# Performance work log

Measured on AMD Instinct MI355X. Metric: run time of the kernel, lower is better.

Reference implementation:

```python
import jax, jax.numpy as jnp
import numpy as np

EPS_LN = 1e-6


def _ln(x):
    m = jnp.mean(x, axis=-1, keepdims=True)
    v = jnp.mean((x - m) ** 2, axis=-1, keepdims=True)
    return (x - m) * jax.lax.rsqrt(v + EPS_LN)


def _rope(q, cos, sin):
    # q: [B,S,H,D]; cos/sin: [S, D//2]; rotate interleaved pairs
    q2 = q.reshape(q.shape[:-1] + (-1, 2))
    a, b = q2[..., 0], q2[..., 1]
    c = cos[None, :, None, :]
    s = sin[None, :, None, :]
    return jnp.stack([a * c - b * s, a * s + b * c], axis=-1).reshape(q.shape)


def _attn(q, k, v):
    # q:[B,Sq,H,D] k,v:[B,Sk,H,D] -> [B,Sq,H,D]; flash default scale 1/sqrt(D)
    D = q.shape[-1]
    scores = jnp.einsum('bqhd,bkhd->bhqk', q, k) / jnp.sqrt(jnp.asarray(D, q.dtype))
    p = jax.nn.softmax(scores, axis=-1)
    return jnp.einsum('bhqk,bkhd->bqhd', p, v)


def setup_inputs() -> dict:
    key = jax.random.key(0)
    C, H, S, T, B = 2048, 16, 1024, 256, 4
    Dh = C // H
    F = int(C * 4)
    L, Ly = B * S, B * T
    ks = jax.random.split(key, 24)

    def w(k, shape):
        return (jax.random.normal(k, shape, dtype=jnp.float32) * 0.02)

    # RoPE angle table: positions 0..S-1 with standard inverse frequencies
    inv_freq = 1.0 / (10000.0 ** (np.arange(0, Dh, 2, dtype=np.float32) / Dh))
    freqs = jnp.asarray(np.arange(S, dtype=np.float32)[:, None] * inv_freq[None, :])

    inp = {
        'x': jax.random.normal(ks[0], (L, C), dtype=jnp.float32),
        'y': jax.random.normal(ks[1], (Ly, C), dtype=jnp.float32),
        't': jax.random.normal(ks[2], (L, 6 * C), dtype=jnp.float32),
        'freqs': freqs,
        'scale_shift_table': jax.random.normal(ks[3], (6, C), dtype=jnp.float32) / (C ** 0.5),
        'Wq_s': w(ks[4], (C, C)), 'bq_s': jnp.zeros((C,), jnp.float32),
        'Wk_s': w(ks[5], (C, C)), 'bk_s': jnp.zeros((C,), jnp.float32),
        'Wv_s': w(ks[6], (C, C)), 'bv_s': jnp.zeros((C,), jnp.float32),
        'Wo_s': w(ks[7], (C, C)), 'bo_s': jnp.zeros((C,), jnp.float32),
        'Wq_c': w(ks[8], (C, C)), 'bq_c': jnp.zeros((C,), jnp.float32),
        'Wk_c': w(ks[9], (C, C)), 'bk_c': jnp.zeros((C,), jnp.float32),
        'Wv_c': w(ks[10], (C, C)), 'bv_c': jnp.zeros((C,), jnp.float32),
        'Wo_c': w(ks[11], (C, C)), 'bo_c': jnp.zeros((C,), jnp.float32),
        'W_fc1': w(ks[12], (F, C)), 'b_fc1': jnp.zeros((F,), jnp.float32),
        'W_fc2': w(ks[13], (C, F)), 'b_fc2': jnp.zeros((C,), jnp.float32),
        'seq_len': S,
        'txt_len': T,
    }
    return inp


def reference(x, y, t, freqs, scale_shift_table,
              Wq_s, bq_s, Wk_s, bk_s, Wv_s, bv_s, Wo_s, bo_s,
              Wq_c, bq_c, Wk_c, bk_c, Wv_c, bv_c, Wo_c, bo_c,
              W_fc1, b_fc1, W_fc2, b_fc2, seq_len, txt_len):
    L, C = x.shape
    Dh = 2 * freqs.shape[1]
    H = C // Dh
    B = L // seq_len
    cos, sin = jnp.cos(freqs), jnp.sin(freqs)

    # per-token AdaLN params (B here == total tokens in torch code)
    mods = scale_shift_table[None] + t.reshape(L, 6, C)
    shift_msa, scale_msa, gate_msa, shift_mlp, scale_mlp, gate_mlp = (
        mods[:, i, :] for i in range(6))

    # ---- self attention (AdaLN modulate + RoPE) ----
    xm = _ln(x) * (1.0 + scale_msa) + shift_msa
    q = (xm @ Wq_s.T + bq_s).reshape(B, seq_len, H, Dh)
    k = (xm @ Wk_s.T + bk_s).reshape(B, seq_len, H, Dh)
    v = (xm @ Wv_s.T + bv_s).reshape(B, seq_len, H, Dh)
    q = _rope(q, cos, sin)
    k = _rope(k, cos, sin)
    a = _attn(q, k, v).reshape(L, C)
    x = x + gate_msa * (a @ Wo_s.T + bo_s)

    # ---- cross attention (no norm/modulation/gate, no RoPE) ----
    q = (x @ Wq_c.T + bq_c).reshape(B, seq_len, H, Dh)
    k = (y @ Wk_c.T + bk_c).reshape(B, txt_len, H, Dh)
    v = (y @ Wv_c.T + bv_c).reshape(B, txt_len, H, Dh)
    a = _attn(q, k, v).reshape(L, C)
    x = x + (a @ Wo_c.T + bo_c)

    # ---- MLP with AdaLN modulate + gate ----
    xm = _ln(x) * (1.0 + scale_mlp) + shift_mlp
    h = jax.nn.gelu(xm @ W_fc1.T + b_fc1, approximate=True)
    x = x + gate_mlp * (h @ W_fc2.T + b_fc2)
    return x
```

## Files before the change

### kernel.cpp

```cpp
#include <hip/hip_runtime.h>
#include <stdint.h>

#define C_DIM 2048
#define H_NUM 16
#define DH    128
#define S_LEN 1024
#define T_LEN 256
#define B_SZ  4
#define L_ROWS 4096
#define LY_ROWS 1024
#define F_DIM 8192

typedef __attribute__((ext_vector_type(4))) float f32x4;
typedef __attribute__((ext_vector_type(8))) __bf16 bf16x8;
typedef __attribute__((ext_vector_type(4))) unsigned short us4;
typedef __attribute__((ext_vector_type(8))) unsigned short us8;
typedef unsigned short u16;

__device__ __forceinline__ u16 f2bf(float f) {
  union { float f; uint32_t u; } v; v.f = f;
  uint32_t r = v.u + 0x7FFFu + ((v.u >> 16) & 1u);
  return (u16)(r >> 16);
}
__device__ __forceinline__ float bf2f(u16 h) {
  union { uint32_t u; float f; } v; v.u = ((uint32_t)h) << 16;
  return v.f;
}

typedef __attribute__((address_space(1))) void gvoid;
typedef __attribute__((address_space(3))) void lvoid;
__device__ __forceinline__ void gl_lds16(const void* g, void* l) {
  __builtin_amdgcn_global_load_lds((gvoid*)g, (lvoid*)l, 16, 0, 0);
}

template<int N> __device__ __forceinline__ void wait_vmcnt() {
  if constexpr (N == 0) asm volatile("s_waitcnt vmcnt(0)" ::: "memory");
  else if constexpr (N == 5) asm volatile("s_waitcnt vmcnt(5)" ::: "memory");
  else if constexpr (N == 6) asm volatile("s_waitcnt vmcnt(6)" ::: "memory");
}
__device__ __forceinline__ void barrier_raw() {
  asm volatile("s_barrier" ::: "memory");
}
__device__ __forceinline__ void lgkm0_pin() {
  asm volatile("s_waitcnt lgkmcnt(0)" ::: "memory");
  __builtin_amdgcn_sched_barrier(0);
}

__global__ void k_cvt(const float* __restrict__ src, u16* __restrict__ dst, int n) {
  int i = (blockIdx.x * blockDim.x + threadIdx.x) * 4;
  int stride = gridDim.x * blockDim.x * 4;
  for (; i < n; i += stride) {
    float4 v = *(const float4*)(src + i);
    us4 o;
    o[0] = f2bf(v.x); o[1] = f2bf(v.y); o[2] = f2bf(v.z); o[3] = f2bf(v.w);
    *(us4*)(dst + i) = o;
  }
}

__global__ __launch_bounds__(256)
void k_modln(const float* __restrict__ x, const float* __restrict__ t,
             const float* __restrict__ tab, u16* __restrict__ out,
             int scale_idx, int shift_idx) {
  int row = blockIdx.x;
  int tid = threadIdx.x;
  const float* xr = x + (size_t)row * C_DIM;
  int c0 = tid * 8;
  float4 a = *(const float4*)(xr + c0);
  float4 b = *(const float4*)(xr + c0 + 4);
  float v[8] = {a.x, a.y, a.z, a.w, b.x, b.y, b.z, b.w};
  float s = 0.f, ss = 0.f;
#pragma unroll
  for (int j = 0; j < 8; ++j) { s += v[j]; ss += v[j] * v[j]; }
#pragma unroll
  for (int m = 1; m < 64; m <<= 1) { s += __shfl_xor(s, m); ss += __shfl_xor(ss, m); }
  __shared__ float red[8];
  int wid = tid >> 6;
  if ((tid & 63) == 0) { red[wid * 2] = s; red[wid * 2 + 1] = ss; }
  __syncthreads();
  s  = red[0] + red[2] + red[4] + red[6];
  ss = red[1] + red[3] + red[5] + red[7];
  float mean = s * (1.f / C_DIM);
  float var  = ss * (1.f / C_DIM) - mean * mean;
  float rstd = rsqrtf(var + 1e-6f);
  const float* trow = t + (size_t)row * (6 * C_DIM);
  const float* tsc = trow + scale_idx * C_DIM + c0;
  const float* tsh = trow + shift_idx * C_DIM + c0;
  const float* gsc = tab + scale_idx * C_DIM + c0;
  const float* gsh = tab + shift_idx * C_DIM + c0;
  us8 o;
#pragma unroll
  for (int j = 0; j < 8; ++j) {
    float scv = 1.f + gsc[j] + tsc[j];
    float shv = gsh[j] + tsh[j];
    o[j] = f2bf((v[j] - mean) * rstd * scv + shv);
  }
  *(us8*)(out + (size_t)row * C_DIM + c0) = o;
}

template<int BM, int EPI>
__global__ __launch_bounds__(512, 2)
void k_gemm3(const u16* __restrict__ A, const u16* __restrict__ W,
             const float* __restrict__ bias0, const float* __restrict__ bias1,
             const float* __restrict__ bias2,
             u16* __restrict__ o0, u16* __restrict__ o1, u16* __restrict__ o2,
             int sec_shift, int out_ld,
             float* __restrict__ outF, const float* __restrict__ resid,
             const float* __restrict__ gate_t, const float* __restrict__ gate_tab,
             int M, int N, int K, int nbx) {
  constexpr int HTA = (BM / 2) * 64;
  constexpr int HTB = 128 * 64;
  constexpr int ACALLS = BM / 128;
  constexpr int QM = BM / 64;
  constexpr int MFR = BM / 32;
  constexpr int VMN = 4 + ACALLS;
  constexpr int BOFF = 4 * HTA;
  __shared__ __align__(16) u16 lds[BOFF + 4 * HTB];

  int tid = threadIdx.x;
  int nwg = gridDim.x;
  int q8 = nwg >> 3, r8 = nwg & 7;
  int xcd = blockIdx.x & 7, local = blockIdx.x >> 3;
  int wgid = (xcd < r8 ? xcd * (q8 + 1) : r8 * (q8 + 1) + (xcd - r8) * q8) + local;
  int bx = wgid % nbx, by = wgid / nbx;
  int m0 = by * BM, n0 = bx * 256;

  int wid = tid >> 6, lane = tid & 63;
  int wm = wid >> 2, wn = wid & 3;
  int lr = lane & 15, lg = lane >> 4;
  int xorslot = ((lr >> 2) & 3) << 1;
  int bcol = (wn & 1) * 64;

  int tsw = tid ^ (((tid >> 5) & 1) << 1) ^ (((tid >> 6) & 1) << 2);
  int srow = tsw >> 3;
  int scol = (tsw & 7) * 8;

  auto stA = [&](int h, int kt2) {
    int pt = kt2 & 1;
    u16* dst = lds + (pt * 2 + h) * HTA + tid * 8;
#pragma unroll
    for (int call = 0; call < ACALLS; ++call) {
      int grow = m0 + h * (BM / 2) + call * 64 + srow;
      gl_lds16(A + (size_t)grow * K + kt2 * 64 + scol, dst + call * 4096);
    }
  };
  auto stB = [&](int h, int kt2) {
    int pt = kt2 & 1;
    u16* dst = lds + BOFF + (pt * 2 + h) * HTB + tid * 8;
#pragma unroll
    for (int call = 0; call < 2; ++call) {
      int grow = n0 + h * 128 + call * 64 + srow;
      gl_lds16(W + (size_t)grow * K + kt2 * 64 + scol, dst + call * 4096);
    }
  };

  f32x4 zero4 = {0.f, 0.f, 0.f, 0.f};
  f32x4 acc[MFR][4];
#pragma unroll
  for (int m = 0; m < MFR; ++m)
#pragma unroll
    for (int n = 0; n < 4; ++n) acc[m][n] = zero4;

  int NT2 = K >> 6;
  stA(0, 0); stA(1, 0); stB(0, 0); stB(1, 0);
  stB(0, 1); stB(1, 1); stA(0, 1);
  wait_vmcnt<VMN>();
  barrier_raw();

  for (int kt = 0; kt < NT2; ++kt) {
    int p = kt & 1;
    const u16* Ah = lds + (p * 2 + wm) * HTA;
    const u16* Bh = lds + BOFF + (p * 2 + (wn >> 1)) * HTB;
    bf16x8 aR[QM][2], bR0[2][2], bR1[2][2];
    bool st1 = (kt + 1) < NT2, st2 = (kt + 2) < NT2;

#pragma unroll
    for (int m = 0; m < QM; ++m) {
      int r = m * 16 + lr;
#pragma unroll
      for (int kk = 0; kk < 2; ++kk)
        aR[m][kk] = *(const bf16x8*)(Ah + r * 64 + (((kk << 2) | lg) ^ xorslot) * 8);
    }
#pragma unroll
    for (int n = 0; n < 2; ++n) {
      int r = bcol + n * 16 + lr;
#pragma unroll
      for (int kk = 0; kk < 2; ++kk)
        bR0[n][kk] = *(const bf16x8*)(Bh + r * 64 + (((kk << 2) | lg) ^ xorslot) * 8);
    }
    if (st1) stA(1, kt + 1);
    lgkm0_pin();
    __builtin_amdgcn_s_setprio(1);
#pragma unroll
    for (int kk = 0; kk < 2; ++kk)
#pragma unroll
      for (int m = 0; m < QM; ++m)
#pragma unroll
        for (int n = 0; n < 2; ++n)
          acc[m][n] = __builtin_amdgcn_mfma_f32_16x16x32_bf16(aR[m][kk], bR0[n][kk], acc[m][n], 0, 0, 0);
    __builtin_amdgcn_s_setprio(0);
    barrier_raw();

#pragma unroll
    for (int n = 0; n < 2; ++n) {
      int r = bcol + 32 + n * 16 + lr;
#pragma unroll
      for (int kk = 0; kk < 2; ++kk)
        bR1[n][kk] = *(const bf16x8*)(Bh + r * 64 + (((kk << 2) | lg) ^ xorslot) * 8);
    }
    lgkm0_pin();
    __builtin_amdgcn_s_setprio(1);
#pragma unroll
    for (int kk = 0; kk < 2; ++kk)
#pragma unroll
      for (int m = 0; m < QM; ++m)
#pragma unroll
        for (int n = 0; n < 2; ++n)
          acc[m][2 + n] = __builtin_amdgcn_mfma_f32_16x16x32_bf16(aR[m][kk], bR1[n][kk], acc[m][2 + n], 0, 0, 0);
    __builtin_amdgcn_s_setprio(0);
    barrier_raw();

#pragma unroll
    for (int m = 0; m < QM; ++m) {
      int r = (BM / 4) + m * 16 + lr;
#pragma unroll
      for (int kk = 0; kk < 2; ++kk)
        aR[m][kk] = *(const bf16x8*)(Ah + r * 64 + (((kk << 2) | lg) ^ xorslot) * 8);
    }
    if (st2) { stB(0, kt + 2); stB(1, kt + 2); }
    lgkm0_pin();
    __builtin_amdgcn_s_setprio(1);
#pragma unroll
    for (int kk = 0; kk < 2; ++kk)
#pragma unroll
      for (int m = 0; m < QM; ++m)
#pragma unroll
        for (int n = 0; n < 2; ++n)
          acc[QM + m][2 + n] = __builtin_amdgcn_mfma_f32_16x16x32_bf16(aR[m][kk], bR1[n][kk], acc[QM + m][2 + n], 0, 0, 0);
    __builtin_amdgcn_s_setprio(0);
    barrier_raw();

    if (st2) stA(0, kt + 2);
    __builtin_amdgcn_s_setprio(1);
#pragma unroll
    for (int kk = 0; kk < 2; ++kk)
#pragma unroll
      for (int m = 0; m < QM; ++m)
#pragma unroll
        for (int n = 0; n < 2; ++n)
          acc[QM + m][n] = __builtin_amdgcn_mfma_f32_16x16x32_bf16(aR[m][kk], bR0[n][kk], acc[QM + m][n], 0, 0, 0);
    __builtin_amdgcn_s_setprio(0);
    if (st2) wait_vmcnt<VMN>(); else wait_vmcnt<0>();
    barrier_raw();
  }

#pragma unroll
  for (int mf = 0; mf < MFR; ++mf) {
    int row0 = m0 + wm * (BM / 2) + mf * 16 + lg * 4;
#pragma unroll
    for (int nf = 0; nf < 4; ++nf) {
      int col = n0 + wn * 64 + nf * 16 + lr;
      if constexpr (EPI == 0) {
        int sec = col >> sec_shift;
        const float* bp = sec == 0 ? bias0 : (sec == 1 ? bias1 : bias2);
        u16* op = sec == 0 ? o0 : (sec == 1 ? o1 : o2);
        int cs = col & ((1 << sec_shift) - 1);
        float bv = bp[cs];
#pragma unroll
        for (int r = 0; r < 4; ++r)
          op[(size_t)(row0 + r) * out_ld + cs] = f2bf(acc[mf][nf][r] + bv);
      } else if constexpr (EPI == 1) {
        float bv = bias0[col];
#pragma unroll
        for (int r = 0; r < 4; ++r) {
          float val = acc[mf][nf][r] + bv;
          float x3 = val * val * val;
          float g = 0.5f * val * (1.f + tanhf(0.7978845608f * (val + 0.044715f * x3)));
          o0[(size_t)(row0 + r) * out_ld + col] = f2bf(g);
        }
      } else if constexpr (EPI == 2) {
        float bv = bias0[col];
        float gt = gate_tab[col];
#pragma unroll
        for (int r = 0; r < 4; ++r) {
          int row = row0 + r;
          size_t idx = (size_t)row * N + col;
          float g = gt + gate_t[(size_t)row * (6 * C_DIM) + col];
          float o = resid[idx] + g * (acc[mf][nf][r] + bv);
          outF[idx] = o;
          if (o0) o0[idx] = f2bf(o);
        }
      } else {
        float bv = bias0[col];
#pragma unroll
        for (int r = 0; r < 4; ++r) {
          size_t idx = (size_t)(row0 + r) * N + col;
          outF[idx] = resid[idx] + (acc[mf][nf][r] + bv);
        }
      }
    }
  }
}

__global__ void k_rope(u16* __restrict__ q, u16* __restrict__ k,
                       const float* __restrict__ freqs) {
  int idx = blockIdx.x * blockDim.x + threadIdx.x;
  int total = L_ROWS * C_DIM / 8;
  for (; idx < total; idx += gridDim.x * blockDim.x) {
    int e = idx * 8;
    int row = e >> 11;
    int col = e & (C_DIM - 1);
    int s = row & (S_LEN - 1);
    int i0 = (col & (DH - 1)) >> 1;
    float4 fr = *(const float4*)(freqs + s * (DH / 2) + i0);
    float cs[4], sn[4];
    float fv[4] = {fr.x, fr.y, fr.z, fr.w};
#pragma unroll
    for (int j = 0; j < 4; ++j) sincosf(fv[j], &sn[j], &cs[j]);
    us8 qa = *(us8*)(q + e);
    us8 ka = *(us8*)(k + e);
#pragma unroll
    for (int p = 0; p < 4; ++p) {
      float a = bf2f(qa[2 * p]), b = bf2f(qa[2 * p + 1]);
      qa[2 * p]     = f2bf(a * cs[p] - b * sn[p]);
      qa[2 * p + 1] = f2bf(a * sn[p] + b * cs[p]);
      float a2 = bf2f(ka[2 * p]), b2 = bf2f(ka[2 * p + 1]);
      ka[2 * p]     = f2bf(a2 * cs[p] - b2 * sn[p]);
      ka[2 * p + 1] = f2bf(a2 * sn[p] + b2 * cs[p]);
    }
    *(us8*)(q + e) = qa;
    *(us8*)(k + e) = ka;
  }
}

__global__ void k_transpose_v(const u16* __restrict__ v, u16* __restrict__ vt, int Lkv) {
  __shared__ u16 tile[32][33];
  int bh = blockIdx.x, b = bh >> 4, h = bh & 15;
  int k0 = blockIdx.y * 32, d0 = blockIdx.z * 32;
  int tx = threadIdx.x, ty = threadIdx.y;
  const u16* src = v + (size_t)(b * Lkv) * C_DIM + h * DH;
#pragma unroll
  for (int j = 0; j < 32; j += 8)
    tile[ty + j][tx] = src[(size_t)(k0 + ty + j) * C_DIM + d0 + tx];
  __syncthreads();
  u16* dst = vt + (size_t)bh * DH * Lkv;
#pragma unroll
  for (int j = 0; j < 32; j += 8)
    dst[(size_t)(d0 + ty + j) * Lkv + k0 + tx] = tile[tx][ty + j];
}

__global__ __launch_bounds__(256)
void k_flash(const u16* __restrict__ Q, const u16* __restrict__ K,
             const u16* __restrict__ Vt, u16* __restrict__ O,
             int Lq, int Lkv, float scale) {
  __shared__ __align__(16) u16 lK[64 * 128];
  __shared__ __align__(16) u16 lV[128 * 64];
  __shared__ __align__(16) u16 lP[4][16 * 72];
  int bh = blockIdx.x, b = bh >> 4, h = bh & 15;
  int tid = threadIdx.x, wid = tid >> 6, lane = tid & 63;
  int lr = lane & 15, lg = lane >> 4;
  int q0 = blockIdx.y * 64 + wid * 16;
  const u16* Qb = Q + ((size_t)(b * Lq) + q0) * C_DIM + h * DH;
  const u16* Kb = K + (size_t)(b * Lkv) * C_DIM + h * DH;
  const u16* Vb = Vt + (size_t)bh * DH * Lkv;

  bf16x8 qf[4];
#pragma unroll
  for (int ks = 0; ks < 4; ++ks)
    qf[ks] = *(const bf16x8*)(Qb + (size_t)lr * C_DIM + ks * 32 + lg * 8);

  f32x4 zero4 = {0.f, 0.f, 0.f, 0.f};
  f32x4 o[8];
#pragma unroll
  for (int n = 0; n < 8; ++n) o[n] = zero4;
  float mrow[4] = {-3.0e38f, -3.0e38f, -3.0e38f, -3.0e38f};
  float lrow[4] = {0.f, 0.f, 0.f, 0.f};

  int nsteps = Lkv >> 6;
  for (int kt = 0; kt < nsteps; ++kt) {
#pragma unroll
    for (int i = 0; i < 4; ++i) {
      int flat = i * 4096 + tid * 16;
      int key = flat >> 8, inner = flat & 255;
      int ksrc = inner ^ ((key & 7) << 4);
      gl_lds16((const char*)Kb + ((size_t)(kt * 64 + key) * C_DIM) * 2 + ksrc, (char*)lK + flat);
      int d = flat >> 7, keyb = flat & 127;
      int vsrc = keyb ^ ((d & 7) << 4);
      gl_lds16((const char*)Vb + ((size_t)d * Lkv) * 2 + kt * 128 + vsrc, (char*)lV + flat);
    }
    __syncthreads();

    f32x4 sc[4];
#pragma unroll
    for (int c = 0; c < 4; ++c) sc[c] = zero4;
#pragma unroll
    for (int c = 0; c < 4; ++c) {
      int key = c * 16 + lr;
#pragma unroll
      for (int ks = 0; ks < 4; ++ks) {
        int off = (ks * 64 + lg * 16) ^ ((key & 7) << 4);
        bf16x8 kf = *(const bf16x8*)((const char*)lK + key * 256 + off);
        sc[c] = __builtin_amdgcn_mfma_f32_16x16x32_bf16(qf[ks], kf, sc[c], 0, 0, 0);
      }
    }
#pragma unroll
    for (int r = 0; r < 4; ++r) {
      float s0 = sc[0][r] * scale, s1 = sc[1][r] * scale;
      float s2 = sc[2][r] * scale, s3 = sc[3][r] * scale;
      float mx = fmaxf(fmaxf(s0, s1), fmaxf(s2, s3));
#pragma unroll
      for (int m = 1; m < 16; m <<= 1) mx = fmaxf(mx, __shfl_xor(mx, m));
      float mnew = fmaxf(mrow[r], mx);
      float alpha = exp2f((mrow[r] - mnew) * 1.44269504f);
      mrow[r] = mnew;
      float p0 = exp2f((s0 - mnew) * 1.44269504f);
      float p1 = exp2f((s1 - mnew) * 1.44269504f);
      float p2 = exp2f((s2 - mnew) * 1.44269504f);
      float p3 = exp2f((s3 - mnew) * 1.44269504f);
      float psum = p0 + p1 + p2 + p3;
#pragma unroll
      for (int m = 1; m < 16; m <<= 1) psum += __shfl_xor(psum, m);
      lrow[r] = lrow[r] * alpha + psum;
#pragma unroll
      for (int n = 0; n < 8; ++n) o[n][r] *= alpha;
      u16* pr = lP[wid] + (4 * lg + r) * 72;
      pr[lr]      = f2bf(p0);
      pr[16 + lr] = f2bf(p1);
      pr[32 + lr] = f2bf(p2);
      pr[48 + lr] = f2bf(p3);
    }
    asm volatile("s_waitcnt lgkmcnt(0)" ::: "memory");
    __builtin_amdgcn_sched_barrier(0);
#pragma unroll
    for (int half = 0; half < 2; ++half) {
      bf16x8 pf = *(const bf16x8*)(lP[wid] + lr * 72 + half * 32 + lg * 8);
#pragma unroll
      for (int n = 0; n < 8; ++n) {
        int d = n * 16 + lr;
        int off = (half * 64 + lg * 16) ^ ((d & 7) << 4);
        bf16x8 vf = *(const bf16x8*)((const char*)lV + d * 128 + off);
        o[n] = __builtin_amdgcn_mfma_f32_16x16x32_bf16(pf, vf, o[n], 0, 0, 0);
      }
    }
    __syncthreads();
  }

  u16* Ob = O + ((size_t)(b * Lq) + q0) * C_DIM + h * DH;
#pragma unroll
  for (int n = 0; n < 8; ++n) {
    int d = n * 16 + lr;
#pragma unroll
    for (int r = 0; r < 4; ++r) {
      int qr = 4 * lg + r;
      Ob[(size_t)qr * C_DIM + d] = f2bf(o[n][r] / lrow[r]);
    }
  }
}

extern "C" void kernel_launch(void* const* d_in, const int* in_sizes, int n_in,
                              void* d_out, int out_size, void* d_ws, size_t ws_size,
                              hipStream_t stream) {
  const float* x     = (const float*)d_in[0];
  const float* y     = (const float*)d_in[1];
  const float* t     = (const float*)d_in[2];
  const float* freqs = (const float*)d_in[3];
  const float* tab   = (const float*)d_in[4];
  const float* Wq_s = (const float*)d_in[5];
  const float* bq_s = (const float*)d_in[6];
  const float* Wk_s = (const float*)d_in[7];
  const float* bk_s = (const float*)d_in[8];
  const float* Wv_s = (const float*)d_in[9];
  const float* bv_s = (const float*)d_in[10];
  const float* Wo_s = (const float*)d_in[11];
  const float* bo_s = (const float*)d_in[12];
  const float* Wq_c = (const float*)d_in[13];
  const float* bq_c = (const float*)d_in[14];
  const float* Wk_c = (const float*)d_in[15];
  const float* bk_c = (const float*)d_in[16];
  const float* Wv_c = (const float*)d_in[17];
  const float* bv_c = (const float*)d_in[18];
  const float* Wo_c = (const float*)d_in[19];
  const float* bo_c = (const float*)d_in[20];
  const float* W_fc1 = (const float*)d_in[21];
  const float* b_fc1 = (const float*)d_in[22];
  const float* W_fc2 = (const float*)d_in[23];
  const float* b_fc2 = (const float*)d_in[24];

  const size_t SZ_CC  = (size_t)C_DIM * C_DIM * 2;
  const size_t SZ_FC  = (size_t)F_DIM * C_DIM * 2;
  const size_t SZ_LC  = (size_t)L_ROWS * C_DIM * 2;
  const size_t SZ_YC  = (size_t)LY_ROWS * C_DIM * 2;
  char* ws = (char*)d_ws;
  size_t off = 0;
  u16* wq_s = (u16*)(ws + off); off += SZ_CC;
  u16* wk_s = (u16*)(ws + off); off += SZ_CC;
  u16* wv_s = (u16*)(ws + off); off += SZ_CC;
  u16* wo_s = (u16*)(ws + off); off += SZ_CC;
  u16* wq_c = (u16*)(ws + off); off += SZ_CC;
  u16* wk_c = (u16*)(ws + off); off += SZ_CC;
  u16* wv_c = (u16*)(ws + off); off += SZ_CC;
  u16* wo_c = (u16*)(ws + off); off += SZ_CC;
  u16* wfc1 = (u16*)(ws + off); off += SZ_FC;
  u16* wfc2 = (u16*)(ws + off); off += SZ_FC;
  u16* ybf  = (u16*)(ws + off); off += SZ_YC;
  u16* xm   = (u16*)(ws + off); off += SZ_LC;
  u16* qb   = (u16*)(ws + off); off += SZ_LC;
  u16* kb   = (u16*)(ws + off); off += SZ_LC;
  u16* vb   = (u16*)(ws + off); off += SZ_LC;
  u16* ao   = (u16*)(ws + off); off += SZ_LC;
  u16* hbuf = qb;
  float* x1 = (float*)(ws + off); off += (size_t)L_ROWS * C_DIM * 4;
  u16* x1bf = (u16*)(ws + off); off += SZ_LC;
  u16* kc   = (u16*)(ws + off); off += SZ_YC;
  u16* vc   = (u16*)(ws + off); off += SZ_YC;
  u16* vt   = (u16*)(ws + off); off += SZ_LC;
  u16* vtc  = (u16*)(ws + off); off += SZ_YC;
  if (ws_size < off) return;

  auto cvt = [&](const float* s, u16* d, int n) {
    int blocks = (n / 4 + 255) / 256; if (blocks > 4096) blocks = 4096;
    k_cvt<<<blocks, 256, 0, stream>>>(s, d, n);
  };
  cvt(Wq_s, wq_s, C_DIM * C_DIM);
  cvt(Wk_s, wk_s, C_DIM * C_DIM);
  cvt(Wv_s, wv_s, C_DIM * C_DIM);
  cvt(Wo_s, wo_s, C_DIM * C_DIM);
  cvt(Wq_c, wq_c, C_DIM * C_DIM);
  cvt(Wk_c, wk_c, C_DIM * C_DIM);
  cvt(Wv_c, wv_c, C_DIM * C_DIM);
  cvt(Wo_c, wo_c, C_DIM * C_DIM);
  cvt(W_fc1, wfc1, F_DIM * C_DIM);
  cvt(W_fc2, wfc2, F_DIM * C_DIM);
  cvt(y, ybf, LY_ROWS * C_DIM);

  const float ascale = 0.08838834764831845f;

  k_modln<<<L_ROWS, 256, 0, stream>>>(x, t, tab, xm, 1, 0);
  k_gemm3<128, 0><<<32 * 24, 512, 0, stream>>>(
      xm, wq_s, bq_s, bk_s, bv_s, qb, kb, vb, 11, C_DIM,
      nullptr, nullptr, nullptr, nullptr, L_ROWS, 6144, C_DIM, 24);
  k_rope<<<2048, 256, 0, stream>>>(qb, kb, freqs);
  k_transpose_v<<<dim3(B_SZ * H_NUM, S_LEN / 32, DH / 32), dim3(32, 8), 0, stream>>>(vb, vt, S_LEN);
  k_flash<<<dim3(B_SZ * H_NUM, S_LEN / 64), 256, 0, stream>>>(qb, kb, vt, ao, S_LEN, S_LEN, ascale);
  k_gemm3<128, 2><<<32 * 8, 512, 0, stream>>>(
      ao, wo_s, bo_s, nullptr, nullptr, x1bf, nullptr, nullptr, 30, C_DIM,
      x1, x, t + 2 * C_DIM, tab + 2 * C_DIM, L_ROWS, C_DIM, C_DIM, 8);
  k_gemm3<128, 0><<<32 * 8, 512, 0, stream>>>(
      x1bf, wq_c, bq_c, nullptr, nullptr, qb, nullptr, nullptr, 30, C_DIM,
      nullptr, nullptr, nullptr, nullptr, L_ROWS, C_DIM, C_DIM, 8);
  k_gemm3<128, 0><<<8 * 16, 512, 0, stream>>>(
      ybf, wk_c, bk_c, bv_c, bv_c, kc, vc, vc, 11, C_DIM,
      nullptr, nullptr, nullptr, nullptr, LY_ROWS, 4096, C_DIM, 16);
  k_transpose_v<<<dim3(B_SZ * H_NUM, T_LEN / 32, DH / 32), dim3(32, 8), 0, stream>>>(vc, vtc, T_LEN);
  k_flash<<<dim3(B_SZ * H_NUM, S_LEN / 64), 256, 0, stream>>>(qb, kc, vtc, ao, S_LEN, T_LEN, ascale);
  k_gemm3<128, 3><<<32 * 8, 512, 0, stream>>>(
      ao, wo_c, bo_c, nullptr, nullptr, nullptr, nullptr, nullptr, 30, C_DIM,
      x1, x1, nullptr, nullptr, L_ROWS, C_DIM, C_DIM, 8);
  k_modln<<<L_ROWS, 256, 0, stream>>>(x1, t, tab, xm, 4, 3);
  k_gemm3<256, 1><<<16 * 32, 512, 0, stream>>>(
      xm, wfc1, b_fc1, nullptr, nullptr, hbuf, nullptr, nullptr, 30, F_DIM,
      nullptr, nullptr, nullptr, nullptr, L_ROWS, F_DIM, C_DIM, 32);
  k_gemm3<128, 2><<<32 * 8, 512, 0, stream>>>(
      hbuf, wfc2, b_fc2, nullptr, nullptr, nullptr, nullptr, nullptr, 30, C_DIM,
      (float*)d_out, x1, t + 5 * C_DIM, tab + 5 * C_DIM, L_ROWS, C_DIM, F_DIM, 8);
}
```

Baseline: 947.5 us.

## Split FC2 GEMM along K into two passes and change the LDS swizzle

```diff
diff --git a/kernel.cpp b/kernel.cpp
--- a/kernel.cpp
+++ b/kernel.cpp
@@ -106,7 +106,8 @@
              int sec_shift, int out_ld,
              float* __restrict__ outF, const float* __restrict__ resid,
              const float* __restrict__ gate_t, const float* __restrict__ gate_tab,
-             int M, int N, int K, int nbx) {
+             const float* __restrict__ partial,
+             int M, int N, int K, int lda, int ldw, int nbx) {
   constexpr int HTA = (BM / 2) * 64;
   constexpr int HTB = 128 * 64;
   constexpr int ACALLS = BM / 128;
@@ -127,12 +128,11 @@
   int wid = tid >> 6, lane = tid & 63;
   int wm = wid >> 2, wn = wid & 3;
   int lr = lane & 15, lg = lane >> 4;
-  int xorslot = ((lr >> 2) & 3) << 1;
+  int xorslot = lr & 7;
   int bcol = (wn & 1) * 64;
 
-  int tsw = tid ^ (((tid >> 5) & 1) << 1) ^ (((tid >> 6) & 1) << 2);
-  int srow = tsw >> 3;
-  int scol = (tsw & 7) * 8;
+  int srow = tid >> 3;
+  int scol = ((tid ^ (tid >> 3)) & 7) * 8;
 
   auto stA = [&](int h, int kt2) {
     int pt = kt2 & 1;
@@ -140,7 +140,7 @@
 #pragma unroll
     for (int call = 0; call < ACALLS; ++call) {
       int grow = m0 + h * (BM / 2) + call * 64 + srow;
-      gl_lds16(A + (size_t)grow * K + kt2 * 64 + scol, dst + call * 4096);
+      gl_lds16(A + (size_t)grow * lda + kt2 * 64 + scol, dst + call * 4096);
     }
   };
   auto stB = [&](int h, int kt2) {
@@ -149,7 +149,7 @@
 #pragma unroll
     for (int call = 0; call < 2; ++call) {
       int grow = n0 + h * 128 + call * 64 + srow;
-      gl_lds16(W + (size_t)grow * K + kt2 * 64 + scol, dst + call * 4096);
+      gl_lds16(W + (size_t)grow * ldw + kt2 * 64 + scol, dst + call * 4096);
     }
   };
 
@@ -178,14 +178,14 @@
       int r = m * 16 + lr;
 #pragma unroll
       for (int kk = 0; kk < 2; ++kk)
-        aR[m][kk] = *(const bf16x8*)(Ah + r * 64 + (((kk << 2) | lg) ^ xorslot) * 8);
+        aR[m][kk] = *(const bf16x8*)(Ah + r * 64 + ((((kk << 2) | lg) ^ xorslot)) * 8);
     }
 #pragma unroll
     for (int n = 0; n < 2; ++n) {
       int r = bcol + n * 16 + lr;
 #pragma unroll
       for (int kk = 0; kk < 2; ++kk)
-        bR0[n][kk] = *(const bf16x8*)(Bh + r * 64 + (((kk << 2) | lg) ^ xorslot) * 8);
+        bR0[n][kk] = *(const bf16x8*)(Bh + r * 64 + ((((kk << 2) | lg) ^ xorslot)) * 8);
     }
     if (st1) stA(1, kt + 1);
     lgkm0_pin();
@@ -205,7 +205,7 @@
       int r = bcol + 32 + n * 16 + lr;
 #pragma unroll
       for (int kk = 0; kk < 2; ++kk)
-        bR1[n][kk] = *(const bf16x8*)(Bh + r * 64 + (((kk << 2) | lg) ^ xorslot) * 8);
+        bR1[n][kk] = *(const bf16x8*)(Bh + r * 64 + ((((kk << 2) | lg) ^ xorslot)) * 8);
     }
     lgkm0_pin();
     __builtin_amdgcn_s_setprio(1);
@@ -224,7 +224,7 @@
       int r = (BM / 4) + m * 16 + lr;
 #pragma unroll
       for (int kk = 0; kk < 2; ++kk)
-        aR[m][kk] = *(const bf16x8*)(Ah + r * 64 + (((kk << 2) | lg) ^ xorslot) * 8);
+        aR[m][kk] = *(const bf16x8*)(Ah + r * 64 + ((((kk << 2) | lg) ^ xorslot)) * 8);
     }
     if (st2) { stB(0, kt + 2); stB(1, kt + 2); }
     lgkm0_pin();
@@ -289,12 +289,27 @@
           outF[idx] = o;
           if (o0) o0[idx] = f2bf(o);
         }
-      } else {
+      } else if constexpr (EPI == 3) {
         float bv = bias0[col];
 #pragma unroll
         for (int r = 0; r < 4; ++r) {
           size_t idx = (size_t)(row0 + r) * N + col;
           outF[idx] = resid[idx] + (acc[mf][nf][r] + bv);
+        }
+      } else if constexpr (EPI == 4) {
+#pragma unroll
+        for (int r = 0; r < 4; ++r)
+          outF[(size_t)(row0 + r) * N + col] = acc[mf][nf][r];
+      } else {
+        float bv = bias0[col];
+        float gt = gate_tab[col];
+#pragma unroll
+        for (int r = 0; r < 4; ++r) {
+          int row = row0 + r;
+          size_t idx = (size_t)row * N + col;
+          float val = acc[mf][nf][r] + partial[idx] + bv;
+          float g = gt + gate_t[(size_t)row * (6 * C_DIM) + col];
+          outF[idx] = resid[idx] + g * val;
         }
       }
     }
@@ -514,6 +529,7 @@
   u16* vc   = (u16*)(ws + off); off += SZ_YC;
   u16* vt   = (u16*)(ws + off); off += SZ_LC;
   u16* vtc  = (u16*)(ws + off); off += SZ_YC;
+  float* part = (float*)x1bf;
   if (ws_size < off) return;
 
   auto cvt = [&](const float* s, u16* d, int n) {
@@ -537,29 +553,33 @@
   k_modln<<<L_ROWS, 256, 0, stream>>>(x, t, tab, xm, 1, 0);
   k_gemm3<128, 0><<<32 * 24, 512, 0, stream>>>(
       xm, wq_s, bq_s, bk_s, bv_s, qb, kb, vb, 11, C_DIM,
-      nullptr, nullptr, nullptr, nullptr, L_ROWS, 6144, C_DIM, 24);
+      nullptr, nullptr, nullptr, nullptr, nullptr, L_ROWS, 6144, C_DIM, C_DIM, C_DIM, 24);
   k_rope<<<2048, 256, 0, stream>>>(qb, kb, freqs);
   k_transpose_v<<<dim3(B_SZ * H_NUM, S_LEN / 32, DH / 32), dim3(32, 8), 0, stream>>>(vb, vt, S_LEN);
   k_flash<<<dim3(B_SZ * H_NUM, S_LEN / 64), 256, 0, stream>>>(qb, kb, vt, ao, S_LEN, S_LEN, ascale);
   k_gemm3<128, 2><<<32 * 8, 512, 0, stream>>>(
       ao, wo_s, bo_s, nullptr, nullptr, x1bf, nullptr, nullptr, 30, C_DIM,
-      x1, x, t + 2 * C_DIM, tab + 2 * C_DIM, L_ROWS, C_DIM, C_DIM, 8);
+      x1, x, t + 2 * C_DIM, tab + 2 * C_DIM, nullptr, L_ROWS, C_DIM, C_DIM, C_DIM, C_DIM, 8);
   k_gemm3<128, 0><<<32 * 8, 512, 0, stream>>>(
       x1bf, wq_c, bq_c, nullptr, nullptr, qb, nullptr, nullptr, 30, C_DIM,
-      nullptr, nullptr, nullptr, nullptr, L_ROWS, C_DIM, C_DIM, 8);
+      nullptr, nullptr, nullptr, nullptr, nullptr, L_ROWS, C_DIM, C_DIM, C_DIM, C_DIM, 8);
   k_gemm3<128, 0><<<8 * 16, 512, 0, stream>>>(
       ybf, wk_c, bk_c, bv_c, bv_c, kc, vc, vc, 11, C_DIM,
-      nullptr, nullptr, nullptr, nullptr, LY_ROWS, 4096, C_DIM, 16);
+      nullptr, nullptr, nullptr, nullptr, nullptr, LY_ROWS, 4096, C_DIM, C_DIM, C_DIM, 16);
   k_transpose_v<<<dim3(B_SZ * H_NUM, T_LEN / 32, DH / 32), dim3(32, 8), 0, stream>>>(vc, vtc, T_LEN);
   k_flash<<<dim3(B_SZ * H_NUM, S_LEN / 64), 256, 0, stream>>>(qb, kc, vtc, ao, S_LEN, T_LEN, ascale);
   k_gemm3<128, 3><<<32 * 8, 512, 0, stream>>>(
       ao, wo_c, bo_c, nullptr, nullptr, nullptr, nullptr, nullptr, 30, C_DIM,
-      x1, x1, nullptr, nullptr, L_ROWS, C_DIM, C_DIM, 8);
+      x1, x1, nullptr, nullptr, nullptr, L_ROWS, C_DIM, C_DIM, C_DIM, C_DIM, 8);
   k_modln<<<L_ROWS, 256, 0, stream>>>(x1, t, tab, xm, 4, 3);
   k_gemm3<256, 1><<<16 * 32, 512, 0, stream>>>(
       xm, wfc1, b_fc1, nullptr, nullptr, hbuf, nullptr, nullptr, 30, F_DIM,
-      nullptr, nullptr, nullptr, nullptr, L_ROWS, F_DIM, C_DIM, 32);
-  k_gemm3<128, 2><<<32 * 8, 512, 0, stream>>>(
-      hbuf, wfc2, b_fc2, nullptr, nullptr, nullptr, nullptr, nullptr, 30, C_DIM,
-      (float*)d_out, x1, t + 5 * C_DIM, tab + 5 * C_DIM, L_ROWS, C_DIM, F_DIM, 8);
-}
+      nullptr, nullptr, nullptr, nullptr, nullptr, L_ROWS, F_DIM, C_DIM, C_DIM, C_DIM, 32);
+  k_gemm3<128, 4><<<32 * 8, 512, 0, stream>>>(
+      hbuf, wfc2, nullptr, nullptr, nullptr, nullptr, nullptr, nullptr, 30, C_DIM,
+      part, nullptr, nullptr, nullptr, nullptr, L_ROWS, C_DIM, F_DIM / 2, F_DIM, F_DIM, 8);
+  k_gemm3<128, 5><<<32 * 8, 512, 0, stream>>>(
+      hbuf + F_DIM / 2, wfc2 + F_DIM / 2, b_fc2, nullptr, nullptr, nullptr, nullptr, nullptr, 30, C_DIM,
+      (float*)d_out, x1, t + 5 * C_DIM, tab + 5 * C_DIM, part,
+      L_ROWS, C_DIM, F_DIM / 2, F_DIM, F_DIM, 8);
+}
```

Measured after the change: 917.9 us. 3.1% less time.

## Add 256x256 GEMM kernel with finer-grained load/MFMA interleaving for QKV and FC1

Applied to the files above, without the earlier changes.

```diff
diff --git a/kernel.cpp b/kernel.cpp
--- a/kernel.cpp
+++ b/kernel.cpp
@@ -35,6 +35,7 @@
 
 template<int N> __device__ __forceinline__ void wait_vmcnt() {
   if constexpr (N == 0) asm volatile("s_waitcnt vmcnt(0)" ::: "memory");
+  else if constexpr (N == 4) asm volatile("s_waitcnt vmcnt(4)" ::: "memory");
   else if constexpr (N == 5) asm volatile("s_waitcnt vmcnt(5)" ::: "memory");
   else if constexpr (N == 6) asm volatile("s_waitcnt vmcnt(6)" ::: "memory");
 }
@@ -97,6 +98,189 @@
   *(us8*)(out + (size_t)row * C_DIM + c0) = o;
 }
 
+template<int EPI>
+__global__ __launch_bounds__(512, 2)
+void k_gemm5(const u16* __restrict__ A, const u16* __restrict__ W,
+             const float* __restrict__ bias0, const float* __restrict__ bias1,
+             const float* __restrict__ bias2,
+             u16* __restrict__ o0, u16* __restrict__ o1, u16* __restrict__ o2,
+             int sec_shift, int out_ld,
+             int M, int N, int K, int lda, int ldw, int nbx) {
+  __shared__ __align__(16) u16 lds[65536];
+
+  int tid = threadIdx.x;
+  int nwg = gridDim.x;
+  int q8 = nwg >> 3, r8 = nwg & 7;
+  int xcd = blockIdx.x & 7, local = blockIdx.x >> 3;
+  int wgid = (xcd < r8 ? xcd * (q8 + 1) : r8 * (q8 + 1) + (xcd - r8) * q8) + local;
+  int bx = wgid % nbx, by = wgid / nbx;
+  int m0 = by * 256, n0 = bx * 256;
+
+  int wid = tid >> 6, lane = tid & 63;
+  int wm = wid >> 2, wn = wid & 3;
+  int lr = lane & 15, lg = lane >> 4;
+  int xorslot = lr & 7;
+  int bcol = (wn & 1) * 64;
+
+  int srow = tid >> 3;
+  int scol = ((tid ^ (tid >> 3)) & 7) * 8;
+
+  auto stA = [&](int buf, int h, int kt) {
+    u16* dst = lds + (buf * 2 + h) * 8192 + tid * 8;
+#pragma unroll
+    for (int call = 0; call < 2; ++call) {
+      int grow = m0 + h * 128 + call * 64 + srow;
+      gl_lds16(A + (size_t)grow * lda + kt * 64 + scol, dst + call * 4096);
+    }
+  };
+  auto stB = [&](int buf, int h, int kt) {
+    u16* dst = lds + 32768 + (buf * 2 + h) * 8192 + tid * 8;
+#pragma unroll
+    for (int call = 0; call < 2; ++call) {
+      int grow = n0 + h * 128 + call * 64 + srow;
+      gl_lds16(W + (size_t)grow * ldw + kt * 64 + scol, dst + call * 4096);
+    }
+  };
+
+  f32x4 zero4 = {0.f, 0.f, 0.f, 0.f};
+  f32x4 acc[8][4];
+#pragma unroll
+  for (int m = 0; m < 8; ++m)
+#pragma unroll
+    for (int n = 0; n < 4; ++n) acc[m][n] = zero4;
+
+  int NT = K >> 6, NJ = NT >> 1;
+  stA(0, 0, 0); stA(0, 1, 0); stB(0, 0, 0); stB(0, 1, 0);
+  stB(1, 0, 1); stA(1, 0, 1);
+  wait_vmcnt<4>();
+  barrier_raw();
+
+  for (int j = 0; j < NJ; ++j) {
+    bool nlast = (j + 1 < NJ);
+    int t1 = 2 * j + 1, t2 = 2 * j + 2, t3 = 2 * j + 3;
+#pragma unroll
+    for (int buf = 0; buf < 2; ++buf) {
+      const u16* Ah = lds + (buf * 2 + wm) * 8192;
+      const u16* Bh = lds + 32768 + (buf * 2 + (wn >> 1)) * 8192;
+      bf16x8 aR[4][2], b0[2][2], b1[2][2];
+
+#pragma unroll
+      for (int m = 0; m < 4; ++m) {
+        int r = m * 16 + lr;
+#pragma unroll
+        for (int kk = 0; kk < 2; ++kk)
+          aR[m][kk] = *(const bf16x8*)(Ah + r * 64 + (((kk << 2) | lg) ^ xorslot) * 8);
+      }
+#pragma unroll
+      for (int n = 0; n < 2; ++n) {
+        int r = bcol + n * 16 + lr;
+#pragma unroll
+        for (int kk = 0; kk < 2; ++kk)
+          b0[n][kk] = *(const bf16x8*)(Bh + r * 64 + (((kk << 2) | lg) ^ xorslot) * 8);
+      }
+      if (buf == 0) stA(1, 1, t1);
+      else if (nlast) stA(0, 1, t2);
+      barrier_raw();
+      lgkm0_pin();
+      __builtin_amdgcn_s_setprio(1);
+#pragma unroll
+      for (int kk = 0; kk < 2; ++kk)
+#pragma unroll
+        for (int m = 0; m < 4; ++m)
+#pragma unroll
+          for (int n = 0; n < 2; ++n)
+            acc[m][n] = __builtin_amdgcn_mfma_f32_16x16x32_bf16(aR[m][kk], b0[n][kk], acc[m][n], 0, 0, 0);
+      __builtin_amdgcn_s_setprio(0);
+      barrier_raw();
+
+#pragma unroll
+      for (int n = 0; n < 2; ++n) {
+        int r = bcol + 32 + n * 16 + lr;
+#pragma unroll
+        for (int kk = 0; kk < 2; ++kk)
+          b1[n][kk] = *(const bf16x8*)(Bh + r * 64 + (((kk << 2) | lg) ^ xorslot) * 8);
+      }
+      if (buf == 0) stB(1, 1, t1);
+      else if (nlast) stB(0, 1, t2);
+      barrier_raw();
+      lgkm0_pin();
+      __builtin_amdgcn_s_setprio(1);
+#pragma unroll
+      for (int kk = 0; kk < 2; ++kk)
+#pragma unroll
+        for (int m = 0; m < 4; ++m)
+#pragma unroll
+          for (int n = 0; n < 2; ++n)
+            acc[m][2 + n] = __builtin_amdgcn_mfma_f32_16x16x32_bf16(aR[m][kk], b1[n][kk], acc[m][2 + n], 0, 0, 0);
+      __builtin_amdgcn_s_setprio(0);
+      barrier_raw();
+
+#pragma unroll
+      for (int m = 0; m < 4; ++m) {
+        int r = 64 + m * 16 + lr;
+#pragma unroll
+        for (int kk = 0; kk < 2; ++kk)
+          aR[m][kk] = *(const bf16x8*)(Ah + r * 64 + (((kk << 2) | lg) ^ xorslot) * 8);
+      }
+      if (nlast) { if (buf == 0) stB(0, 0, t2); else stB(1, 0, t3); }
+      barrier_raw();
+      lgkm0_pin();
+      __builtin_amdgcn_s_setprio(1);
+#pragma unroll
+      for (int kk = 0; kk < 2; ++kk)
+#pragma unroll
+        for (int m = 0; m < 4; ++m)
+#pragma unroll
+          for (int n = 0; n < 2; ++n)
+            acc[4 + m][2 + n] = __builtin_amdgcn_mfma_f32_16x16x32_bf16(aR[m][kk], b1[n][kk], acc[4 + m][2 + n], 0, 0, 0);
+      __builtin_amdgcn_s_setprio(0);
+      barrier_raw();
+
+      if (nlast) { if (buf == 0) stA(0, 0, t2); else stA(1, 0, t3); }
+      barrier_raw();
+      __builtin_amdgcn_s_setprio(1);
+#pragma unroll
+      for (int kk = 0; kk < 2; ++kk)
+#pragma unroll
+        for (int m = 0; m < 4; ++m)
+#pragma unroll
+          for (int n = 0; n < 2; ++n)
+            acc[4 + m][n] = __builtin_amdgcn_mfma_f32_16x16x32_bf16(aR[m][kk], b0[n][kk], acc[4 + m][n], 0, 0, 0);
+      __builtin_amdgcn_s_setprio(0);
+      if (nlast) wait_vmcnt<4>(); else wait_vmcnt<0>();
+      barrier_raw();
+    }
+  }
+
+#pragma unroll
+  for (int mf = 0; mf < 8; ++mf) {
+    int row0 = m0 + wm * 128 + mf * 16 + lg * 4;
+#pragma unroll
+    for (int nf = 0; nf < 4; ++nf) {
+      int col = n0 + wn * 64 + nf * 16 + lr;
+      if constexpr (EPI == 0) {
+        int sec = col >> sec_shift;
+        const float* bp = sec == 0 ? bias0 : (sec == 1 ? bias1 : bias2);
+        u16* op = sec == 0 ? o0 : (sec == 1 ? o1 : o2);
+        int cs = col & ((1 << sec_shift) - 1);
+        float bv = bp[cs];
+#pragma unroll
+        for (int r = 0; r < 4; ++r)
+          op[(size_t)(row0 + r) * out_ld + cs] = f2bf(acc[mf][nf][r] + bv);
+      } else {
+        float bv = bias0[col];
+#pragma unroll
+        for (int r = 0; r < 4; ++r) {
+          float val = acc[mf][nf][r] + bv;
+          float x3 = val * val * val;
+          float g = 0.5f * val * (1.f + tanhf(0.7978845608f * (val + 0.044715f * x3)));
+          o0[(size_t)(row0 + r) * out_ld + col] = f2bf(g);
+        }
+      }
+    }
+  }
+}
+
 template<int BM, int EPI>
 __global__ __launch_bounds__(512, 2)
 void k_gemm3(const u16* __restrict__ A, const u16* __restrict__ W,
@@ -106,7 +290,7 @@
              int sec_shift, int out_ld,
              float* __restrict__ outF, const float* __restrict__ resid,
              const float* __restrict__ gate_t, const float* __restrict__ gate_tab,
-             int M, int N, int K, int nbx) {
+             int M, int N, int K, int lda, int ldw, int nbx) {
   constexpr int HTA = (BM / 2) * 64;
   constexpr int HTB = 128 * 64;
   constexpr int ACALLS = BM / 128;
@@ -127,12 +311,11 @@
   int wid = tid >> 6, lane = tid & 63;
   int wm = wid >> 2, wn = wid & 3;
   int lr = lane & 15, lg = lane >> 4;
-  int xorslot = ((lr >> 2) & 3) << 1;
+  int xorslot = lr & 7;
   int bcol = (wn & 1) * 64;
 
-  int tsw = tid ^ (((tid >> 5) & 1) << 1) ^ (((tid >> 6) & 1) << 2);
-  int srow = tsw >> 3;
-  int scol = (tsw & 7) * 8;
+  int srow = tid >> 3;
+  int scol = ((tid ^ (tid >> 3)) & 7) * 8;
 
   auto stA = [&](int h, int kt2) {
     int pt = kt2 & 1;
@@ -140,7 +323,7 @@
 #pragma unroll
     for (int call = 0; call < ACALLS; ++call) {
       int grow = m0 + h * (BM / 2) + call * 64 + srow;
-      gl_lds16(A + (size_t)grow * K + kt2 * 64 + scol, dst + call * 4096);
+      gl_lds16(A + (size_t)grow * lda + kt2 * 64 + scol, dst + call * 4096);
     }
   };
   auto stB = [&](int h, int kt2) {
@@ -149,7 +332,7 @@
 #pragma unroll
     for (int call = 0; call < 2; ++call) {
       int grow = n0 + h * 128 + call * 64 + srow;
-      gl_lds16(W + (size_t)grow * K + kt2 * 64 + scol, dst + call * 4096);
+      gl_lds16(W + (size_t)grow * ldw + kt2 * 64 + scol, dst + call * 4096);
     }
   };
 
@@ -268,15 +451,6 @@
 #pragma unroll
         for (int r = 0; r < 4; ++r)
           op[(size_t)(row0 + r) * out_ld + cs] = f2bf(acc[mf][nf][r] + bv);
-      } else if constexpr (EPI == 1) {
-        float bv = bias0[col];
-#pragma unroll
-        for (int r = 0; r < 4; ++r) {
-          float val = acc[mf][nf][r] + bv;
-          float x3 = val * val * val;
-          float g = 0.5f * val * (1.f + tanhf(0.7978845608f * (val + 0.044715f * x3)));
-          o0[(size_t)(row0 + r) * out_ld + col] = f2bf(g);
-        }
       } else if constexpr (EPI == 2) {
         float bv = bias0[col];
         float gt = gate_tab[col];
@@ -535,31 +709,31 @@
   const float ascale = 0.08838834764831845f;
 
   k_modln<<<L_ROWS, 256, 0, stream>>>(x, t, tab, xm, 1, 0);
-  k_gemm3<128, 0><<<32 * 24, 512, 0, stream>>>(
+  k_gemm5<0><<<16 * 24, 512, 0, stream>>>(
       xm, wq_s, bq_s, bk_s, bv_s, qb, kb, vb, 11, C_DIM,
-      nullptr, nullptr, nullptr, nullptr, L_ROWS, 6144, C_DIM, 24);
+      L_ROWS, 6144, C_DIM, C_DIM, C_DIM, 24);
   k_rope<<<2048, 256, 0, stream>>>(qb, kb, freqs);
   k_transpose_v<<<dim3(B_SZ * H_NUM, S_LEN / 32, DH / 32), dim3(32, 8), 0, stream>>>(vb, vt, S_LEN);
   k_flash<<<dim3(B_SZ * H_NUM, S_LEN / 64), 256, 0, stream>>>(qb, kb, vt, ao, S_LEN, S_LEN, ascale);
   k_gemm3<128, 2><<<32 * 8, 512, 0, stream>>>(
       ao, wo_s, bo_s, nullptr, nullptr, x1bf, nullptr, nullptr, 30, C_DIM,
-      x1, x, t + 2 * C_DIM, tab + 2 * C_DIM, L_ROWS, C_DIM, C_DIM, 8);
+      x1, x, t + 2 * C_DIM, tab + 2 * C_DIM, L_ROWS, C_DIM, C_DIM, C_DIM, C_DIM, 8);
   k_gemm3<128, 0><<<32 * 8, 512, 0, stream>>>(
       x1bf, wq_c, bq_c, nullptr, nullptr, qb, nullptr, nullptr, 30, C_DIM,
-      nullptr, nullptr, nullptr, nullptr, L_ROWS, C_DIM, C_DIM, 8);
+      nullptr, nullptr, nullptr, nullptr, L_ROWS, C_DIM, C_DIM, C_DIM, C_DIM, 8);
   k_gemm3<128, 0><<<8 * 16, 512, 0, stream>>>(
       ybf, wk_c, bk_c, bv_c, bv_c, kc, vc, vc, 11, C_DIM,
-      nullptr, nullptr, nullptr, nullptr, LY_ROWS, 4096, C_DIM, 16);
+      nullptr, nullptr, nullptr, nullptr, LY_ROWS, 4096, C_DIM, C_DIM, C_DIM, 16);
   k_transpose_v<<<dim3(B_SZ * H_NUM, T_LEN / 32, DH / 32), dim3(32, 8), 0, stream>>>(vc, vtc, T_LEN);
   k_flash<<<dim3(B_SZ * H_NUM, S_LEN / 64), 256, 0, stream>>>(qb, kc, vtc, ao, S_LEN, T_LEN, ascale);
   k_gemm3<128, 3><<<32 * 8, 512, 0, stream>>>(
       ao, wo_c, bo_c, nullptr, nullptr, nullptr, nullptr, nullptr, 30, C_DIM,
-      x1, x1, nullptr, nullptr, L_ROWS, C_DIM, C_DIM, 8);
+      x1, x1, nullptr, nullptr, L_ROWS, C_DIM, C_DIM, C_DIM, C_DIM, 8);
   k_modln<<<L_ROWS, 256, 0, stream>>>(x1, t, tab, xm, 4, 3);
-  k_gemm3<256, 1><<<16 * 32, 512, 0, stream>>>(
+  k_gemm5<1><<<16 * 32, 512, 0, stream>>>(
       xm, wfc1, b_fc1, nullptr, nullptr, hbuf, nullptr, nullptr, 30, F_DIM,
-      nullptr, nullptr, nullptr, nullptr, L_ROWS, F_DIM, C_DIM, 32);
+      L_ROWS, F_DIM, C_DIM, C_DIM, C_DIM, 32);
   k_gemm3<128, 2><<<32 * 8, 512, 0, stream>>>(
       hbuf, wfc2, b_fc2, nullptr, nullptr, nullptr, nullptr, nullptr, 30, C_DIM,
-      (float*)d_out, x1, t + 5 * C_DIM, tab + 5 * C_DIM, L_ROWS, C_DIM, F_DIM, 8);
-}
+      (float*)d_out, x1, t + 5 * C_DIM, tab + 5 * C_DIM, L_ROWS, C_DIM, F_DIM, F_DIM, F_DIM, 8);
+}
```

Measured after the change: 922.5 us. 1.03x faster.
